# Optimization experiments

Hardware: AMD Instinct MI355X
Metric: run time of the kernel (lower is better)

The kernel has to match this reference:

```python
import jax, jax.numpy as jnp
import numpy as np

N, E, D, L = 50000, 800000, 128, 3  # nodes, edges, feature dim, layers
BN_EPS = 1e-5


def setup_inputs() -> dict:
    key = jax.random.key(0)
    ks = jax.random.split(key, 6)
    x = jax.random.normal(ks[0], (N, D), dtype=jnp.float32)
    edge_index = jax.random.randint(ks[1], (2, E), 0, N, dtype=jnp.int64)
    eps = jnp.zeros((L,), dtype=jnp.float32)
    # Linear weights ~ fan-in scaled init for numerical sanity
    W1 = jax.random.normal(ks[2], (L, D, D), dtype=jnp.float32) * (1.0 / np.sqrt(D))
    b1 = jnp.zeros((L, D), dtype=jnp.float32)
    W2 = jax.random.normal(ks[3], (L, D, D), dtype=jnp.float32) * (1.0 / np.sqrt(D))
    b2 = jnp.zeros((L, D), dtype=jnp.float32)
    bn1_g = jnp.ones((L, D), dtype=jnp.float32)
    bn1_b = jnp.zeros((L, D), dtype=jnp.float32)
    bn2_g = jnp.ones((L, D), dtype=jnp.float32)
    bn2_b = jnp.zeros((L, D), dtype=jnp.float32)
    return {"x": x, "edge_index": edge_index, "eps": eps, "W1": W1, "b1": b1,
            "bn1_g": bn1_g, "bn1_b": bn1_b, "W2": W2, "b2": b2,
            "bn2_g": bn2_g, "bn2_b": bn2_b}


def _batchnorm(h, g, b):
    # training-mode BatchNorm1d over node axis
    mu = h.mean(axis=0)
    var = h.var(axis=0)
    return (h - mu) * jax.lax.rsqrt(var + BN_EPS) * g + b


def reference(x, edge_index, eps, W1, b1, bn1_g, bn1_b, W2, b2, bn2_g, bn2_b):
    src = edge_index[0]
    dst = edge_index[1]
    h = x
    for l in range(L):
        # message: relu(x_j) gathered per edge; aggregate: scatter-add at dst
        agg = jax.ops.segment_sum(jax.nn.relu(h[src]), dst, num_segments=N)
        z = (1.0 + eps[l]) * h + agg
        # GINConv.mlp: Linear -> BN -> ReLU -> Linear
        z = _batchnorm(z @ W1[l] + b1[l], bn1_g[l], bn1_b[l])
        z = jax.nn.relu(z) @ W2[l] + b2[l]
        # outer per-layer BatchNorm
        z = _batchnorm(z, bn2_g[l], bn2_b[l])
        # ReLU on all but last layer (dropout is identity in eval)
        h = jax.nn.relu(z) if l < L - 1 else z
    return h
```

## Files before the change

kernel.cpp:

```cpp
#include <hip/hip_runtime.h>

#define N_NODES 50000
#define DIM 128
#define BN_EPS 1e-5f

__global__ __launch_bounds__(256) void edge_hist(const int* __restrict__ dst,
                                                 int* __restrict__ cnt, int E) {
  const int e = blockIdx.x * blockDim.x + threadIdx.x;
  if (e < E) atomicAdd(&cnt[dst[e]], 1);
}

__global__ __launch_bounds__(1024) void edge_scan(const int* __restrict__ cnt,
                                                  int* __restrict__ row_ptr) {
  __shared__ int part[1024];
  const int tid = threadIdx.x;
  const int per = (N_NODES + 1023) / 1024;
  const int start = tid * per;
  const int end = min(start + per, N_NODES);
  int s = 0;
  for (int i = start; i < end; ++i) s += cnt[i];
  part[tid] = s;
  __syncthreads();
  for (int off = 1; off < 1024; off <<= 1) {
    const int v = part[tid];
    const int u = (tid >= off) ? part[tid - off] : 0;
    __syncthreads();
    part[tid] = v + u;
    __syncthreads();
  }
  int run = (tid == 0) ? 0 : part[tid - 1];
  for (int i = start; i < end; ++i) {
    row_ptr[i] = run;
    run += cnt[i];
  }
  if (tid == 1023) row_ptr[N_NODES] = run;
}

__global__ __launch_bounds__(256) void edge_fill(const int* __restrict__ src,
                                                 const int* __restrict__ dst,
                                                 const int* __restrict__ row_ptr,
                                                 int* __restrict__ cur,
                                                 int* __restrict__ srcl, int E) {
  const int e = blockIdx.x * blockDim.x + threadIdx.x;
  if (e < E) {
    const int d = dst[e];
    const int pos = row_ptr[d] + atomicAdd(&cur[d], 1);
    srcl[pos] = src[e];
  }
}

template <int FUSE>
__global__ __launch_bounds__(256) void aggregate_combine(
    const float* __restrict__ h, const int* __restrict__ rp,
    const int* __restrict__ srcl, const float* __restrict__ eps_l,
    const float* __restrict__ ac, float* __restrict__ z) {
  const int node =
      __builtin_amdgcn_readfirstlane(blockIdx.x * 4 + (threadIdx.x >> 6));
  if (node >= N_NODES) return;
  const int lane = threadIdx.x & 63;
  const int col = lane * 2;

  float2 av, cv;
  if (FUSE) {
    av.x = ac[col]; av.y = ac[col + 1];
    cv.x = ac[DIM + col]; cv.y = ac[DIM + col + 1];
  }
  const float epsv = 1.0f + *eps_l;

  float2 acc;
  {
    const float2 u =
        *reinterpret_cast<const float2*>(h + (size_t)node * DIM + col);
    float2 s;
    if (FUSE) {
      s.x = fmaxf(fmaf(av.x, u.x, cv.x), 0.f);
      s.y = fmaxf(fmaf(av.y, u.y, cv.y), 0.f);
    } else {
      s = u;
    }
    acc.x = epsv * s.x;
    acc.y = epsv * s.y;
  }

  int p = rp[node];
  const int pe = rp[node + 1];
  for (; p + 8 <= pe; p += 8) {
    int s[8];
#pragma unroll
    for (int i = 0; i < 8; ++i) s[i] = srcl[p + i];
    float2 v[8];
#pragma unroll
    for (int i = 0; i < 8; ++i)
      v[i] = *reinterpret_cast<const float2*>(h + (size_t)s[i] * DIM + col);
#pragma unroll
    for (int i = 0; i < 8; ++i) {
      float mx, my;
      if (FUSE) {
        mx = fmaxf(fmaf(av.x, v[i].x, cv.x), 0.f);
        my = fmaxf(fmaf(av.y, v[i].y, cv.y), 0.f);
      } else {
        mx = fmaxf(v[i].x, 0.f);
        my = fmaxf(v[i].y, 0.f);
      }
      acc.x += mx;
      acc.y += my;
    }
  }
  for (; p < pe; ++p) {
    const int s = srcl[p];
    const float2 v =
        *reinterpret_cast<const float2*>(h + (size_t)s * DIM + col);
    if (FUSE) {
      acc.x += fmaxf(fmaf(av.x, v.x, cv.x), 0.f);
      acc.y += fmaxf(fmaf(av.y, v.y, cv.y), 0.f);
    } else {
      acc.x += fmaxf(v.x, 0.f);
      acc.y += fmaxf(v.y, 0.f);
    }
  }
  *reinterpret_cast<float2*>(z + (size_t)node * DIM + col) = acc;
}

template <int MODE>
__global__ __launch_bounds__(256) void gemm_rw(
    const float* __restrict__ in, const float* __restrict__ ac,
    const float* __restrict__ W, const float* __restrict__ bias,
    float* __restrict__ out, float* __restrict__ stats) {
  const int lane = threadIdx.x & 63;
  const int colb = __builtin_amdgcn_readfirstlane((threadIdx.x >> 6) * 32);
  const int row = blockIdx.x * 64 + lane;
  const bool valid = row < N_NODES;
  const float* __restrict__ zr = in + (size_t)(valid ? row : 0) * DIM;

  float acc[32];
#pragma unroll
  for (int j = 0; j < 32; ++j) acc[j] = 0.f;

#define LDCH(Z0, Z1, CH)                                                    \
  {                                                                         \
    const int kb_ = (CH) * 8;                                               \
    Z0 = *reinterpret_cast<const float4*>(zr + kb_);                        \
    Z1 = *reinterpret_cast<const float4*>(zr + kb_ + 4);                    \
    if (MODE == 1) {                                                        \
      const float4 A0_ = *reinterpret_cast<const float4*>(ac + kb_);        \
      const float4 A1_ = *reinterpret_cast<const float4*>(ac + kb_ + 4);    \
      const float4 C0_ = *reinterpret_cast<const float4*>(ac + DIM + kb_);  \
      const float4 C1_ = *reinterpret_cast<const float4*>(ac + DIM + kb_ + 4); \
      Z0.x = fmaxf(fmaf(A0_.x, Z0.x, C0_.x), 0.f);                          \
      Z0.y = fmaxf(fmaf(A0_.y, Z0.y, C0_.y), 0.f);                          \
      Z0.z = fmaxf(fmaf(A0_.z, Z0.z, C0_.z), 0.f);                          \
      Z0.w = fmaxf(fmaf(A0_.w, Z0.w, C0_.w), 0.f);                          \
      Z1.x = fmaxf(fmaf(A1_.x, Z1.x, C1_.x), 0.f);                          \
      Z1.y = fmaxf(fmaf(A1_.y, Z1.y, C1_.y), 0.f);                          \
      Z1.z = fmaxf(fmaf(A1_.z, Z1.z, C1_.z), 0.f);                          \
      Z1.w = fmaxf(fmaf(A1_.w, Z1.w, C1_.w), 0.f);                          \
    }                                                                       \
  }

#define FMAK(ZK, KG)                                                        \
  {                                                                         \
    const float* __restrict__ wk_ = W + (size_t)(KG)*DIM + colb;            \
    _Pragma("unroll") for (int j = 0; j < 32; ++j) acc[j] =                 \
        fmaf(wk_[j], (ZK), acc[j]);                                         \
  }

#define FMACH(Z0, Z1, CH)                                                   \
  {                                                                         \
    const int kb0_ = (CH) * 8;                                              \
    FMAK(Z0.x, kb0_ + 0) FMAK(Z0.y, kb0_ + 1)                               \
    FMAK(Z0.z, kb0_ + 2) FMAK(Z0.w, kb0_ + 3)                               \
    FMAK(Z1.x, kb0_ + 4) FMAK(Z1.y, kb0_ + 5)                               \
    FMAK(Z1.z, kb0_ + 6) FMAK(Z1.w, kb0_ + 7)                               \
  }

  float4 a0, a1, b0, b1;
  LDCH(a0, a1, 0)
#pragma unroll 1
  for (int c = 0; c < 16; c += 2) {
    LDCH(b0, b1, c + 1)
    FMACH(a0, a1, c)
    if (c + 2 < 16) LDCH(a0, a1, c + 2)
    FMACH(b0, b1, c + 1)
  }
#undef LDCH
#undef FMAK
#undef FMACH

  const float* __restrict__ bb = bias + colb;
  float v[32];
#pragma unroll
  for (int j = 0; j < 32; ++j) v[j] = valid ? (acc[j] + bb[j]) : 0.f;
  if (valid) {
    float* op = out + (size_t)row * DIM + colb;
#pragma unroll
    for (int j4 = 0; j4 < 8; ++j4) {
      float4 o;
      o.x = v[j4 * 4 + 0]; o.y = v[j4 * 4 + 1];
      o.z = v[j4 * 4 + 2]; o.w = v[j4 * 4 + 3];
      *reinterpret_cast<float4*>(op + j4 * 4) = o;
    }
  }
  float q[16];
#pragma unroll
  for (int jj = 0; jj < 16; ++jj) {
    const bool hi = (lane & 32) != 0;
    const float keep = hi ? v[jj + 16] : v[jj];
    const float send = hi ? v[jj] : v[jj + 16];
    const float recv = __shfl_xor(send, 32);
    v[jj] = keep + recv;
    q[jj] = keep * keep + recv * recv;
  }
#define RSTEP(ARR, CNT, O)                                                  \
  {                                                                         \
    _Pragma("unroll") for (int jj = 0; jj < (CNT); ++jj) {                  \
      const bool hi_ = (lane & (O)) != 0;                                   \
      const float keep_ = hi_ ? ARR[jj + (CNT)] : ARR[jj];                  \
      const float send_ = hi_ ? ARR[jj] : ARR[jj + (CNT)];                  \
      ARR[jj] = keep_ + __shfl_xor(send_, (O));                             \
    }                                                                       \
  }
  RSTEP(v, 8, 16) RSTEP(q, 8, 16)
  RSTEP(v, 4, 8)  RSTEP(q, 4, 8)
  RSTEP(v, 2, 4)  RSTEP(q, 2, 4)
  RSTEP(v, 1, 2)  RSTEP(q, 1, 2)
#undef RSTEP
  v[0] += __shfl_xor(v[0], 1);
  q[0] += __shfl_xor(q[0], 1);
  if ((lane & 1) == 0) {
    const int jc = colb + (lane >> 1);
    atomicAdd(&stats[jc], v[0]);
    atomicAdd(&stats[DIM + jc], q[0]);
  }
}

__global__ void bn_param(const float* __restrict__ stats,
                         const float* __restrict__ g,
                         const float* __restrict__ b, float* __restrict__ ac) {
  const int j = threadIdx.x;
  const float invN = 1.0f / (float)N_NODES;
  const float mu = stats[j] * invN;
  const float var = stats[DIM + j] * invN - mu * mu;
  const float a = g[j] * rsqrtf(var + BN_EPS);
  ac[j] = a;
  ac[DIM + j] = b[j] - mu * a;
}

__global__ __launch_bounds__(256) void apply_bn(const float* __restrict__ t,
                                                const float* __restrict__ ac,
                                                float* __restrict__ out) {
  const int i = blockIdx.x * blockDim.x + threadIdx.x;
  const int k = (i * 4) & (DIM - 1);
  const float4 v = *reinterpret_cast<const float4*>(&t[(size_t)i * 4]);
  const float4 a = *reinterpret_cast<const float4*>(&ac[k]);
  const float4 c = *reinterpret_cast<const float4*>(&ac[DIM + k]);
  float4 r;
  r.x = fmaf(a.x, v.x, c.x);
  r.y = fmaf(a.y, v.y, c.y);
  r.z = fmaf(a.z, v.z, c.z);
  r.w = fmaf(a.w, v.w, c.w);
  *reinterpret_cast<float4*>(&out[(size_t)i * 4]) = r;
}

extern "C" void kernel_launch(void* const* d_in, const int* in_sizes, int n_in,
                              void* d_out, int out_size, void* d_ws,
                              size_t ws_size, hipStream_t stream) {
  const float* x = (const float*)d_in[0];
  const int* ei = (const int*)d_in[1];
  const float* eps = (const float*)d_in[2];
  const float* W1 = (const float*)d_in[3];
  const float* b1 = (const float*)d_in[4];
  const float* g1 = (const float*)d_in[5];
  const float* bb1 = (const float*)d_in[6];
  const float* W2 = (const float*)d_in[7];
  const float* b2 = (const float*)d_in[8];
  const float* g2 = (const float*)d_in[9];
  const float* bb2 = (const float*)d_in[10];

  const int E = in_sizes[1] / 2;
  const size_t ND = (size_t)N_NODES * DIM;

  float* bufA = (float*)d_ws;
  float* bufB = bufA + ND;
  float* stats = bufB + ND;
  float* bnp = stats + 512;
  int* cnt = (int*)(bnp + 512);
  int* row_ptr = cnt + N_NODES;
  int* cur = row_ptr + N_NODES + 1;
  int* srcl = cur + N_NODES;

  const int edge_grid = (E + 255) / 256;
  const int agg_grid = (N_NODES + 3) / 4;
  const int gemm_grid = (N_NODES + 63) / 64;
  const int apply_grid = (N_NODES * DIM / 4) / 256;

  hipMemsetAsync(cnt, 0, sizeof(int) * (size_t)N_NODES, stream);
  hipMemsetAsync(cur, 0, sizeof(int) * (size_t)N_NODES, stream);
  edge_hist<<<edge_grid, 256, 0, stream>>>(ei + E, cnt, E);
  edge_scan<<<1, 1024, 0, stream>>>(cnt, row_ptr);
  edge_fill<<<edge_grid, 256, 0, stream>>>(ei, ei + E, row_ptr, cur, srcl, E);

  const float* hin = x;
  float* zb = bufA;
  float* tb = bufB;
  for (int l = 0; l < 3; ++l) {
    hipMemsetAsync(stats, 0, sizeof(float) * 512, stream);
    if (l == 0)
      aggregate_combine<0><<<agg_grid, 256, 0, stream>>>(hin, row_ptr, srcl,
                                                         eps + l, nullptr, zb);
    else
      aggregate_combine<1><<<agg_grid, 256, 0, stream>>>(
          hin, row_ptr, srcl, eps + l, bnp + 256, zb);
    gemm_rw<2><<<gemm_grid, 256, 0, stream>>>(
        zb, nullptr, W1 + (size_t)l * DIM * DIM, b1 + l * DIM, tb, stats);
    bn_param<<<1, DIM, 0, stream>>>(stats, g1 + l * DIM, bb1 + l * DIM, bnp);
    gemm_rw<1><<<gemm_grid, 256, 0, stream>>>(
        tb, bnp, W2 + (size_t)l * DIM * DIM, b2 + l * DIM, zb, stats + 256);
    bn_param<<<1, DIM, 0, stream>>>(stats + 256, g2 + l * DIM, bb2 + l * DIM,
                                    bnp + 256);
    hin = zb;
    float* tmp = zb;
    zb = tb;
    tb = tmp;
  }
  apply_bn<<<apply_grid, 256, 0, stream>>>(hin, bnp + 256, (float*)d_out);
}
```

Before: 883.7 us.

## Stage GEMM weights in LDS and compute two rows per thread

The dense 128x128 GEMM kernel now copies the full weight matrix into shared memory once per block. Each thread computes two output rows (128 rows per block) instead of one, so every weight read from LDS is reused across two rows. The per-column BN statistics reduction is restructured to add the two rows' contributions before the cross-lane shuffle reduction. This is meant to cut the scalar and global weight loads per FMA, at the cost of 64KB LDS per block (lower occupancy) and more registers from two 32-wide accumulators.

After: 1.650 ms. 86.7% more time.

```diff
diff --git a/kernel.cpp b/kernel.cpp
--- a/kernel.cpp
+++ b/kernel.cpp
@@ -122,113 +122,148 @@
 }
 
 template <int MODE>
-__global__ __launch_bounds__(256) void gemm_rw(
+__global__ __launch_bounds__(256) void gemm_v3(
     const float* __restrict__ in, const float* __restrict__ ac,
     const float* __restrict__ W, const float* __restrict__ bias,
     float* __restrict__ out, float* __restrict__ stats) {
-  const int lane = threadIdx.x & 63;
-  const int colb = __builtin_amdgcn_readfirstlane((threadIdx.x >> 6) * 32);
-  const int row = blockIdx.x * 64 + lane;
-  const bool valid = row < N_NODES;
-  const float* __restrict__ zr = in + (size_t)(valid ? row : 0) * DIM;
-
-  float acc[32];
-#pragma unroll
-  for (int j = 0; j < 32; ++j) acc[j] = 0.f;
-
-#define LDCH(Z0, Z1, CH)                                                    \
-  {                                                                         \
-    const int kb_ = (CH) * 8;                                               \
-    Z0 = *reinterpret_cast<const float4*>(zr + kb_);                        \
-    Z1 = *reinterpret_cast<const float4*>(zr + kb_ + 4);                    \
-    if (MODE == 1) {                                                        \
-      const float4 A0_ = *reinterpret_cast<const float4*>(ac + kb_);        \
-      const float4 A1_ = *reinterpret_cast<const float4*>(ac + kb_ + 4);    \
-      const float4 C0_ = *reinterpret_cast<const float4*>(ac + DIM + kb_);  \
-      const float4 C1_ = *reinterpret_cast<const float4*>(ac + DIM + kb_ + 4); \
-      Z0.x = fmaxf(fmaf(A0_.x, Z0.x, C0_.x), 0.f);                          \
-      Z0.y = fmaxf(fmaf(A0_.y, Z0.y, C0_.y), 0.f);                          \
-      Z0.z = fmaxf(fmaf(A0_.z, Z0.z, C0_.z), 0.f);                          \
-      Z0.w = fmaxf(fmaf(A0_.w, Z0.w, C0_.w), 0.f);                          \
-      Z1.x = fmaxf(fmaf(A1_.x, Z1.x, C1_.x), 0.f);                          \
-      Z1.y = fmaxf(fmaf(A1_.y, Z1.y, C1_.y), 0.f);                          \
-      Z1.z = fmaxf(fmaf(A1_.z, Z1.z, C1_.z), 0.f);                          \
-      Z1.w = fmaxf(fmaf(A1_.w, Z1.w, C1_.w), 0.f);                          \
-    }                                                                       \
-  }
-
-#define FMAK(ZK, KG)                                                        \
-  {                                                                         \
-    const float* __restrict__ wk_ = W + (size_t)(KG)*DIM + colb;            \
-    _Pragma("unroll") for (int j = 0; j < 32; ++j) acc[j] =                 \
-        fmaf(wk_[j], (ZK), acc[j]);                                         \
-  }
-
-#define FMACH(Z0, Z1, CH)                                                   \
-  {                                                                         \
-    const int kb0_ = (CH) * 8;                                              \
-    FMAK(Z0.x, kb0_ + 0) FMAK(Z0.y, kb0_ + 1)                               \
-    FMAK(Z0.z, kb0_ + 2) FMAK(Z0.w, kb0_ + 3)                               \
-    FMAK(Z1.x, kb0_ + 4) FMAK(Z1.y, kb0_ + 5)                               \
-    FMAK(Z1.z, kb0_ + 6) FMAK(Z1.w, kb0_ + 7)                               \
-  }
-
-  float4 a0, a1, b0, b1;
-  LDCH(a0, a1, 0)
+  __shared__ float w_lds[DIM * DIM];
+
+  const int tid = threadIdx.x;
+  const int lane = tid & 63;
+  const int colb = __builtin_amdgcn_readfirstlane((tid >> 6) * 32);
+  const int r0 = blockIdx.x * 128 + lane;
+  const int r1 = r0 + 64;
+  const bool v0 = r0 < N_NODES;
+  const bool v1 = r1 < N_NODES;
+  const float* __restrict__ zp0 = in + (size_t)(v0 ? r0 : 0) * DIM;
+  const float* __restrict__ zp1 = in + (size_t)(v1 ? r1 : 0) * DIM;
+
+  float acc0[32], acc1[32];
+#pragma unroll
+  for (int j = 0; j < 32; ++j) { acc0[j] = 0.f; acc1[j] = 0.f; }
+
+#define LOADZ(Z0, Z1, C)                                                     \
+  {                                                                          \
+    const int kb_ = (C) * 16;                                                \
+    _Pragma("unroll") for (int q = 0; q < 4; ++q) {                          \
+      Z0[q] = *reinterpret_cast<const float4*>(zp0 + kb_ + q * 4);           \
+      Z1[q] = *reinterpret_cast<const float4*>(zp1 + kb_ + q * 4);           \
+      if (MODE == 1) {                                                       \
+        const float4 A_ = *reinterpret_cast<const float4*>(ac + kb_ + q * 4);\
+        const float4 C_ =                                                    \
+            *reinterpret_cast<const float4*>(ac + DIM + kb_ + q * 4);        \
+        Z0[q].x = fmaxf(fmaf(A_.x, Z0[q].x, C_.x), 0.f);                     \
+        Z0[q].y = fmaxf(fmaf(A_.y, Z0[q].y, C_.y), 0.f);                     \
+        Z0[q].z = fmaxf(fmaf(A_.z, Z0[q].z, C_.z), 0.f);                     \
+        Z0[q].w = fmaxf(fmaf(A_.w, Z0[q].w, C_.w), 0.f);                     \
+        Z1[q].x = fmaxf(fmaf(A_.x, Z1[q].x, C_.x), 0.f);                     \
+        Z1[q].y = fmaxf(fmaf(A_.y, Z1[q].y, C_.y), 0.f);                     \
+        Z1[q].z = fmaxf(fmaf(A_.z, Z1[q].z, C_.z), 0.f);                     \
+        Z1[q].w = fmaxf(fmaf(A_.w, Z1[q].w, C_.w), 0.f);                     \
+      }                                                                      \
+    }                                                                        \
+  }
+
+#define FMA_K(z0v, z1v, KIDX)                                                \
+  {                                                                          \
+    _Pragma("unroll") for (int jj = 0; jj < 8; ++jj) {                       \
+      const float4 wf_ = *reinterpret_cast<const float4*>(                   \
+          &w_lds[(KIDX) * DIM + colb + jj * 4]);                             \
+      acc0[jj * 4 + 0] = fmaf(wf_.x, (z0v), acc0[jj * 4 + 0]);               \
+      acc0[jj * 4 + 1] = fmaf(wf_.y, (z0v), acc0[jj * 4 + 1]);               \
+      acc0[jj * 4 + 2] = fmaf(wf_.z, (z0v), acc0[jj * 4 + 2]);               \
+      acc0[jj * 4 + 3] = fmaf(wf_.w, (z0v), acc0[jj * 4 + 3]);               \
+      acc1[jj * 4 + 0] = fmaf(wf_.x, (z1v), acc1[jj * 4 + 0]);               \
+      acc1[jj * 4 + 1] = fmaf(wf_.y, (z1v), acc1[jj * 4 + 1]);               \
+      acc1[jj * 4 + 2] = fmaf(wf_.z, (z1v), acc1[jj * 4 + 2]);               \
+      acc1[jj * 4 + 3] = fmaf(wf_.w, (z1v), acc1[jj * 4 + 3]);               \
+    }                                                                        \
+  }
+
+#define COMPUTE(Z0, Z1, C)                                                   \
+  {                                                                          \
+    _Pragma("unroll") for (int q = 0; q < 4; ++q) {                          \
+      const int k0_ = (C) * 16 + q * 4;                                      \
+      FMA_K(Z0[q].x, Z1[q].x, k0_ + 0)                                       \
+      FMA_K(Z0[q].y, Z1[q].y, k0_ + 1)                                       \
+      FMA_K(Z0[q].z, Z1[q].z, k0_ + 2)                                       \
+      FMA_K(Z0[q].w, Z1[q].w, k0_ + 3)                                       \
+    }                                                                        \
+  }
+
+  float4 xa0[4], xa1[4], xb0[4], xb1[4];
+  LOADZ(xa0, xa1, 0)
+
+#pragma unroll
+  for (int it = 0; it < 16; ++it) {
+    const int i4 = it * 256 + tid;
+    *reinterpret_cast<float4*>(&w_lds[i4 * 4]) =
+        *reinterpret_cast<const float4*>(&W[(size_t)i4 * 4]);
+  }
+  __syncthreads();
+
 #pragma unroll 1
-  for (int c = 0; c < 16; c += 2) {
-    LDCH(b0, b1, c + 1)
-    FMACH(a0, a1, c)
-    if (c + 2 < 16) LDCH(a0, a1, c + 2)
-    FMACH(b0, b1, c + 1)
-  }
-#undef LDCH
-#undef FMAK
-#undef FMACH
+  for (int c = 0; c < 8; c += 2) {
+    LOADZ(xb0, xb1, c + 1)
+    COMPUTE(xa0, xa1, c)
+    if (c + 2 < 8) LOADZ(xa0, xa1, c + 2)
+    COMPUTE(xb0, xb1, c + 1)
+  }
+#undef LOADZ
+#undef FMA_K
+#undef COMPUTE
 
   const float* __restrict__ bb = bias + colb;
-  float v[32];
-#pragma unroll
-  for (int j = 0; j < 32; ++j) v[j] = valid ? (acc[j] + bb[j]) : 0.f;
-  if (valid) {
-    float* op = out + (size_t)row * DIM + colb;
+  float s[32], q[32];
+#pragma unroll
+  for (int j = 0; j < 32; ++j) {
+    const float x0 = v0 ? (acc0[j] + bb[j]) : 0.f;
+    const float x1 = v1 ? (acc1[j] + bb[j]) : 0.f;
+    acc0[j] = x0;
+    acc1[j] = x1;
+    s[j] = x0 + x1;
+    q[j] = x0 * x0 + x1 * x1;
+  }
+  if (v0) {
+    float* op = out + (size_t)r0 * DIM + colb;
 #pragma unroll
     for (int j4 = 0; j4 < 8; ++j4) {
       float4 o;
-      o.x = v[j4 * 4 + 0]; o.y = v[j4 * 4 + 1];
-      o.z = v[j4 * 4 + 2]; o.w = v[j4 * 4 + 3];
+      o.x = acc0[j4 * 4 + 0]; o.y = acc0[j4 * 4 + 1];
+      o.z = acc0[j4 * 4 + 2]; o.w = acc0[j4 * 4 + 3];
       *reinterpret_cast<float4*>(op + j4 * 4) = o;
     }
   }
-  float q[16];
-#pragma unroll
-  for (int jj = 0; jj < 16; ++jj) {
-    const bool hi = (lane & 32) != 0;
-    const float keep = hi ? v[jj + 16] : v[jj];
-    const float send = hi ? v[jj] : v[jj + 16];
-    const float recv = __shfl_xor(send, 32);
-    v[jj] = keep + recv;
-    q[jj] = keep * keep + recv * recv;
-  }
-#define RSTEP(ARR, CNT, O)                                                  \
-  {                                                                         \
-    _Pragma("unroll") for (int jj = 0; jj < (CNT); ++jj) {                  \
-      const bool hi_ = (lane & (O)) != 0;                                   \
-      const float keep_ = hi_ ? ARR[jj + (CNT)] : ARR[jj];                  \
-      const float send_ = hi_ ? ARR[jj] : ARR[jj + (CNT)];                  \
-      ARR[jj] = keep_ + __shfl_xor(send_, (O));                             \
-    }                                                                       \
-  }
-  RSTEP(v, 8, 16) RSTEP(q, 8, 16)
-  RSTEP(v, 4, 8)  RSTEP(q, 4, 8)
-  RSTEP(v, 2, 4)  RSTEP(q, 2, 4)
-  RSTEP(v, 1, 2)  RSTEP(q, 1, 2)
+  if (v1) {
+    float* op = out + (size_t)r1 * DIM + colb;
+#pragma unroll
+    for (int j4 = 0; j4 < 8; ++j4) {
+      float4 o;
+      o.x = acc1[j4 * 4 + 0]; o.y = acc1[j4 * 4 + 1];
+      o.z = acc1[j4 * 4 + 2]; o.w = acc1[j4 * 4 + 3];
+      *reinterpret_cast<float4*>(op + j4 * 4) = o;
+    }
+  }
+#define RSTEP(ARR, CNT, O)                                                   \
+  {                                                                          \
+    _Pragma("unroll") for (int jj = 0; jj < (CNT); ++jj) {                   \
+      const bool hi_ = (lane & (O)) != 0;                                    \
+      const float keep_ = hi_ ? ARR[jj + (CNT)] : ARR[jj];                   \
+      const float send_ = hi_ ? ARR[jj] : ARR[jj + (CNT)];                   \
+      ARR[jj] = keep_ + __shfl_xor(send_, (O));                              \
+    }                                                                        \
+  }
+  RSTEP(s, 16, 32) RSTEP(q, 16, 32)
+  RSTEP(s, 8, 16)  RSTEP(q, 8, 16)
+  RSTEP(s, 4, 8)   RSTEP(q, 4, 8)
+  RSTEP(s, 2, 4)   RSTEP(q, 2, 4)
+  RSTEP(s, 1, 2)   RSTEP(q, 1, 2)
 #undef RSTEP
-  v[0] += __shfl_xor(v[0], 1);
+  s[0] += __shfl_xor(s[0], 1);
   q[0] += __shfl_xor(q[0], 1);
   if ((lane & 1) == 0) {
     const int jc = colb + (lane >> 1);
-    atomicAdd(&stats[jc], v[0]);
+    atomicAdd(&stats[jc], s[0]);
     atomicAdd(&stats[DIM + jc], q[0]);
   }
 }
@@ -290,7 +325,7 @@
 
   const int edge_grid = (E + 255) / 256;
   const int agg_grid = (N_NODES + 3) / 4;
-  const int gemm_grid = (N_NODES + 63) / 64;
+  const int gemm_grid = (N_NODES + 127) / 128;
   const int apply_grid = (N_NODES * DIM / 4) / 256;
 
   hipMemsetAsync(cnt, 0, sizeof(int) * (size_t)N_NODES, stream);
@@ -310,10 +345,10 @@
     else
       aggregate_combine<1><<<agg_grid, 256, 0, stream>>>(
           hin, row_ptr, srcl, eps + l, bnp + 256, zb);
-    gemm_rw<2><<<gemm_grid, 256, 0, stream>>>(
+    gemm_v3<2><<<gemm_grid, 256, 0, stream>>>(
         zb, nullptr, W1 + (size_t)l * DIM * DIM, b1 + l * DIM, tb, stats);
     bn_param<<<1, DIM, 0, stream>>>(stats, g1 + l * DIM, bb1 + l * DIM, bnp);
-    gemm_rw<1><<<gemm_grid, 256, 0, stream>>>(
+    gemm_v3<1><<<gemm_grid, 256, 0, stream>>>(
         tb, bnp, W2 + (size_t)l * DIM * DIM, b2 + l * DIM, zb, stats + 256);
     bn_param<<<1, DIM, 0, stream>>>(stats + 256, g2 + l * DIM, bb2 + l * DIM,
                                     bnp + 256);
```

## Replace FP32 FMA GEMM with split-bf16 MFMA GEMM using prepacked weights

Applied to the files above, without the earlier changes.

Swaps the scalar FP32 FMA matrix multiply for one built on the bf16 MFMA 16x16x32 instructions. Precision is kept near FP32 by splitting each operand into bf16 hi and lo parts and issuing three MFMAs (hi*hi, lo*hi, hi*lo). Weights are split and repacked into the MFMA fragment layout by a new prep kernel once per call. The epilogue writes output, adds bias, and accumulates the BatchNorm column sums and squared sums through shuffles and atomics. The cost is three times the MFMA work, a per-element conversion step, and small accuracy differences from the dropped lo*lo term.

New measurement: 834.2 us. 5.6% less time.

```diff
diff --git a/kernel.cpp b/kernel.cpp
--- a/kernel.cpp
+++ b/kernel.cpp
@@ -3,6 +3,18 @@
 #define N_NODES 50000
 #define DIM 128
 #define BN_EPS 1e-5f
+
+typedef short bf16x8 __attribute__((ext_vector_type(8)));
+typedef float f32x4 __attribute__((ext_vector_type(4)));
+
+__device__ __forceinline__ unsigned short f2bf(float x) {
+  unsigned u = __float_as_uint(x);
+  u += 0x7FFFu + ((u >> 16) & 1u);
+  return (unsigned short)(u >> 16);
+}
+__device__ __forceinline__ float bf2f(unsigned short h) {
+  return __uint_as_float(((unsigned)h) << 16);
+}
 
 __global__ __launch_bounds__(256) void edge_hist(const int* __restrict__ dst,
                                                  int* __restrict__ cnt, int E) {
@@ -121,115 +133,144 @@
   *reinterpret_cast<float2*>(z + (size_t)node * DIM + col) = acc;
 }
 
+__global__ __launch_bounds__(256) void prep_w(const float* __restrict__ W,
+                                              unsigned short* __restrict__ hi,
+                                              unsigned short* __restrict__ lo) {
+  const int idx = blockIdx.x * 256 + threadIdx.x;
+  const int i = idx & 7;
+  const int l = (idx >> 3) & 63;
+  const int t = (idx >> 9) & 7;
+  const int s = idx >> 12;
+  const int k = s * 32 + ((l >> 4) << 3) + i;
+  const int j = t * 16 + (l & 15);
+  const float v = W[k * DIM + j];
+  const unsigned short h = f2bf(v);
+  hi[idx] = h;
+  lo[idx] = f2bf(v - bf2f(h));
+}
+
 template <int MODE>
-__global__ __launch_bounds__(256) void gemm_rw(
+__global__ __launch_bounds__(256, 2) void gemm_mfma(
     const float* __restrict__ in, const float* __restrict__ ac,
-    const float* __restrict__ W, const float* __restrict__ bias,
+    const unsigned short* __restrict__ whi,
+    const unsigned short* __restrict__ wlo, const float* __restrict__ bias,
     float* __restrict__ out, float* __restrict__ stats) {
-  const int lane = threadIdx.x & 63;
-  const int colb = __builtin_amdgcn_readfirstlane((threadIdx.x >> 6) * 32);
-  const int row = blockIdx.x * 64 + lane;
-  const bool valid = row < N_NODES;
-  const float* __restrict__ zr = in + (size_t)(valid ? row : 0) * DIM;
-
-  float acc[32];
-#pragma unroll
-  for (int j = 0; j < 32; ++j) acc[j] = 0.f;
-
-#define LDCH(Z0, Z1, CH)                                                    \
-  {                                                                         \
-    const int kb_ = (CH) * 8;                                               \
-    Z0 = *reinterpret_cast<const float4*>(zr + kb_);                        \
-    Z1 = *reinterpret_cast<const float4*>(zr + kb_ + 4);                    \
-    if (MODE == 1) {                                                        \
-      const float4 A0_ = *reinterpret_cast<const float4*>(ac + kb_);        \
-      const float4 A1_ = *reinterpret_cast<const float4*>(ac + kb_ + 4);    \
-      const float4 C0_ = *reinterpret_cast<const float4*>(ac + DIM + kb_);  \
-      const float4 C1_ = *reinterpret_cast<const float4*>(ac + DIM + kb_ + 4); \
-      Z0.x = fmaxf(fmaf(A0_.x, Z0.x, C0_.x), 0.f);                          \
-      Z0.y = fmaxf(fmaf(A0_.y, Z0.y, C0_.y), 0.f);                          \
-      Z0.z = fmaxf(fmaf(A0_.z, Z0.z, C0_.z), 0.f);                          \
-      Z0.w = fmaxf(fmaf(A0_.w, Z0.w, C0_.w), 0.f);                          \
-      Z1.x = fmaxf(fmaf(A1_.x, Z1.x, C1_.x), 0.f);                          \
-      Z1.y = fmaxf(fmaf(A1_.y, Z1.y, C1_.y), 0.f);                          \
-      Z1.z = fmaxf(fmaf(A1_.z, Z1.z, C1_.z), 0.f);                          \
-      Z1.w = fmaxf(fmaf(A1_.w, Z1.w, C1_.w), 0.f);                          \
-    }                                                                       \
-  }
-
-#define FMAK(ZK, KG)                                                        \
-  {                                                                         \
-    const float* __restrict__ wk_ = W + (size_t)(KG)*DIM + colb;            \
-    _Pragma("unroll") for (int j = 0; j < 32; ++j) acc[j] =                 \
-        fmaf(wk_[j], (ZK), acc[j]);                                         \
-  }
-
-#define FMACH(Z0, Z1, CH)                                                   \
-  {                                                                         \
-    const int kb0_ = (CH) * 8;                                              \
-    FMAK(Z0.x, kb0_ + 0) FMAK(Z0.y, kb0_ + 1)                               \
-    FMAK(Z0.z, kb0_ + 2) FMAK(Z0.w, kb0_ + 3)                               \
-    FMAK(Z1.x, kb0_ + 4) FMAK(Z1.y, kb0_ + 5)                               \
-    FMAK(Z1.z, kb0_ + 6) FMAK(Z1.w, kb0_ + 7)                               \
-  }
-
-  float4 a0, a1, b0, b1;
-  LDCH(a0, a1, 0)
+  const int tid = threadIdx.x;
+  const int lane = tid & 63;
+  const int wv = tid >> 6;
+  const int rbase = blockIdx.x * 128 + wv * 32;
+  const int lr = lane & 15;
+  const int lk = (lane >> 4) << 3;
+
+  f32x4 acc[2][8];
+#pragma unroll
+  for (int m = 0; m < 2; ++m)
+#pragma unroll
+    for (int t = 0; t < 8; ++t) acc[m][t] = (f32x4)(0.f);
+
+  const int r0 = min(rbase + lr, N_NODES - 1);
+  const int r1 = min(rbase + 16 + lr, N_NODES - 1);
+  const float* __restrict__ z0 = in + (size_t)r0 * DIM + lk;
+  const float* __restrict__ z1 = in + (size_t)r1 * DIM + lk;
+  const bf16x8* __restrict__ bh = (const bf16x8*)whi + lane;
+  const bf16x8* __restrict__ bl = (const bf16x8*)wlo + lane;
+
 #pragma unroll 1
-  for (int c = 0; c < 16; c += 2) {
-    LDCH(b0, b1, c + 1)
-    FMACH(a0, a1, c)
-    if (c + 2 < 16) LDCH(a0, a1, c + 2)
-    FMACH(b0, b1, c + 1)
-  }
-#undef LDCH
-#undef FMAK
-#undef FMACH
-
-  const float* __restrict__ bb = bias + colb;
-  float v[32];
-#pragma unroll
-  for (int j = 0; j < 32; ++j) v[j] = valid ? (acc[j] + bb[j]) : 0.f;
-  if (valid) {
-    float* op = out + (size_t)row * DIM + colb;
-#pragma unroll
-    for (int j4 = 0; j4 < 8; ++j4) {
-      float4 o;
-      o.x = v[j4 * 4 + 0]; o.y = v[j4 * 4 + 1];
-      o.z = v[j4 * 4 + 2]; o.w = v[j4 * 4 + 3];
-      *reinterpret_cast<float4*>(op + j4 * 4) = o;
-    }
-  }
-  float q[16];
-#pragma unroll
-  for (int jj = 0; jj < 16; ++jj) {
-    const bool hi = (lane & 32) != 0;
-    const float keep = hi ? v[jj + 16] : v[jj];
-    const float send = hi ? v[jj] : v[jj + 16];
-    const float recv = __shfl_xor(send, 32);
-    v[jj] = keep + recv;
-    q[jj] = keep * keep + recv * recv;
-  }
-#define RSTEP(ARR, CNT, O)                                                  \
-  {                                                                         \
-    _Pragma("unroll") for (int jj = 0; jj < (CNT); ++jj) {                  \
-      const bool hi_ = (lane & (O)) != 0;                                   \
-      const float keep_ = hi_ ? ARR[jj + (CNT)] : ARR[jj];                  \
-      const float send_ = hi_ ? ARR[jj] : ARR[jj + (CNT)];                  \
-      ARR[jj] = keep_ + __shfl_xor(send_, (O));                             \
-    }                                                                       \
-  }
-  RSTEP(v, 8, 16) RSTEP(q, 8, 16)
-  RSTEP(v, 4, 8)  RSTEP(q, 4, 8)
-  RSTEP(v, 2, 4)  RSTEP(q, 2, 4)
-  RSTEP(v, 1, 2)  RSTEP(q, 1, 2)
-#undef RSTEP
-  v[0] += __shfl_xor(v[0], 1);
-  q[0] += __shfl_xor(q[0], 1);
-  if ((lane & 1) == 0) {
-    const int jc = colb + (lane >> 1);
-    atomicAdd(&stats[jc], v[0]);
-    atomicAdd(&stats[DIM + jc], q[0]);
+  for (int s = 0; s < 4; ++s) {
+    const int k0 = s * 32;
+    float a0v[8], a1v[8];
+    {
+      const float4 p0 = *reinterpret_cast<const float4*>(z0 + k0);
+      const float4 p1 = *reinterpret_cast<const float4*>(z0 + k0 + 4);
+      a0v[0] = p0.x; a0v[1] = p0.y; a0v[2] = p0.z; a0v[3] = p0.w;
+      a0v[4] = p1.x; a0v[5] = p1.y; a0v[6] = p1.z; a0v[7] = p1.w;
+      const float4 q0 = *reinterpret_cast<const float4*>(z1 + k0);
+      const float4 q1 = *reinterpret_cast<const float4*>(z1 + k0 + 4);
+      a1v[0] = q0.x; a1v[1] = q0.y; a1v[2] = q0.z; a1v[3] = q0.w;
+      a1v[4] = q1.x; a1v[5] = q1.y; a1v[6] = q1.z; a1v[7] = q1.w;
+    }
+    if (MODE == 1) {
+      const float4 A0 = *reinterpret_cast<const float4*>(ac + k0 + lk);
+      const float4 A1 = *reinterpret_cast<const float4*>(ac + k0 + lk + 4);
+      const float4 C0 = *reinterpret_cast<const float4*>(ac + DIM + k0 + lk);
+      const float4 C1 =
+          *reinterpret_cast<const float4*>(ac + DIM + k0 + lk + 4);
+      float aa[8], cc[8];
+      aa[0] = A0.x; aa[1] = A0.y; aa[2] = A0.z; aa[3] = A0.w;
+      aa[4] = A1.x; aa[5] = A1.y; aa[6] = A1.z; aa[7] = A1.w;
+      cc[0] = C0.x; cc[1] = C0.y; cc[2] = C0.z; cc[3] = C0.w;
+      cc[4] = C1.x; cc[5] = C1.y; cc[6] = C1.z; cc[7] = C1.w;
+#pragma unroll
+      for (int i = 0; i < 8; ++i) {
+        a0v[i] = fmaxf(fmaf(aa[i], a0v[i], cc[i]), 0.f);
+        a1v[i] = fmaxf(fmaf(aa[i], a1v[i], cc[i]), 0.f);
+      }
+    }
+    bf16x8 ah0, al0, ah1, al1;
+#pragma unroll
+    for (int i = 0; i < 8; ++i) {
+      unsigned short h = f2bf(a0v[i]);
+      ah0[i] = (short)h;
+      al0[i] = (short)f2bf(a0v[i] - bf2f(h));
+      h = f2bf(a1v[i]);
+      ah1[i] = (short)h;
+      al1[i] = (short)f2bf(a1v[i] - bf2f(h));
+    }
+#pragma unroll
+    for (int t = 0; t < 8; ++t) {
+      const bf16x8 bhv = bh[(s * 8 + t) * 64];
+      const bf16x8 blv = bl[(s * 8 + t) * 64];
+      acc[0][t] =
+          __builtin_amdgcn_mfma_f32_16x16x32_bf16(ah0, bhv, acc[0][t], 0, 0, 0);
+      acc[0][t] =
+          __builtin_amdgcn_mfma_f32_16x16x32_bf16(al0, bhv, acc[0][t], 0, 0, 0);
+      acc[0][t] =
+          __builtin_amdgcn_mfma_f32_16x16x32_bf16(ah0, blv, acc[0][t], 0, 0, 0);
+      acc[1][t] =
+          __builtin_amdgcn_mfma_f32_16x16x32_bf16(ah1, bhv, acc[1][t], 0, 0, 0);
+      acc[1][t] =
+          __builtin_amdgcn_mfma_f32_16x16x32_bf16(al1, bhv, acc[1][t], 0, 0, 0);
+      acc[1][t] =
+          __builtin_amdgcn_mfma_f32_16x16x32_bf16(ah1, blv, acc[1][t], 0, 0, 0);
+    }
+  }
+
+  float bj[8];
+#pragma unroll
+  for (int t = 0; t < 8; ++t) bj[t] = bias[t * 16 + lr];
+  float cs[8], cq[8];
+#pragma unroll
+  for (int t = 0; t < 8; ++t) { cs[t] = 0.f; cq[t] = 0.f; }
+#pragma unroll
+  for (int m = 0; m < 2; ++m) {
+    const int rb2 = rbase + m * 16 + ((lane >> 4) << 2);
+#pragma unroll
+    for (int t = 0; t < 8; ++t) {
+#pragma unroll
+      for (int j = 0; j < 4; ++j) {
+        const int rr = rb2 + j;
+        const float v = acc[m][t][j] + bj[t];
+        if (rr < N_NODES) {
+          out[(size_t)rr * DIM + t * 16 + lr] = v;
+          cs[t] += v;
+          cq[t] += v * v;
+        }
+      }
+    }
+  }
+#pragma unroll
+  for (int t = 0; t < 8; ++t) {
+    cs[t] += __shfl_xor(cs[t], 16);
+    cs[t] += __shfl_xor(cs[t], 32);
+    cq[t] += __shfl_xor(cq[t], 16);
+    cq[t] += __shfl_xor(cq[t], 32);
+  }
+  if (lane < 16) {
+#pragma unroll
+    for (int t = 0; t < 8; ++t) {
+      atomicAdd(&stats[t * 16 + lane], cs[t]);
+      atomicAdd(&stats[DIM + t * 16 + lane], cq[t]);
+    }
   }
 }
 
@@ -287,11 +328,19 @@
   int* row_ptr = cnt + N_NODES;
   int* cur = row_ptr + N_NODES + 1;
   int* srcl = cur + N_NODES;
+  unsigned short* wf = (unsigned short*)(srcl + E);
 
   const int edge_grid = (E + 255) / 256;
   const int agg_grid = (N_NODES + 3) / 4;
-  const int gemm_grid = (N_NODES + 63) / 64;
+  const int gemm_grid = (N_NODES + 127) / 128;
   const int apply_grid = (N_NODES * DIM / 4) / 256;
+
+  for (int l = 0; l < 3; ++l) {
+    unsigned short* f1 = wf + (size_t)(2 * l) * 32768;
+    unsigned short* f2 = wf + (size_t)(2 * l + 1) * 32768;
+    prep_w<<<64, 256, 0, stream>>>(W1 + (size_t)l * DIM * DIM, f1, f1 + 16384);
+    prep_w<<<64, 256, 0, stream>>>(W2 + (size_t)l * DIM * DIM, f2, f2 + 16384);
+  }
 
   hipMemsetAsync(cnt, 0, sizeof(int) * (size_t)N_NODES, stream);
   hipMemsetAsync(cur, 0, sizeof(int) * (size_t)N_NODES, stream);
@@ -303,6 +352,8 @@
   float* zb = bufA;
   float* tb = bufB;
   for (int l = 0; l < 3; ++l) {
+    unsigned short* f1 = wf + (size_t)(2 * l) * 32768;
+    unsigned short* f2 = wf + (size_t)(2 * l + 1) * 32768;
     hipMemsetAsync(stats, 0, sizeof(float) * 512, stream);
     if (l == 0)
       aggregate_combine<0><<<agg_grid, 256, 0, stream>>>(hin, row_ptr, srcl,
@@ -310,11 +361,11 @@
     else
       aggregate_combine<1><<<agg_grid, 256, 0, stream>>>(
           hin, row_ptr, srcl, eps + l, bnp + 256, zb);
-    gemm_rw<2><<<gemm_grid, 256, 0, stream>>>(
-        zb, nullptr, W1 + (size_t)l * DIM * DIM, b1 + l * DIM, tb, stats);
+    gemm_mfma<2><<<gemm_grid, 256, 0, stream>>>(zb, nullptr, f1, f1 + 16384,
+                                                b1 + l * DIM, tb, stats);
     bn_param<<<1, DIM, 0, stream>>>(stats, g1 + l * DIM, bb1 + l * DIM, bnp);
-    gemm_rw<1><<<gemm_grid, 256, 0, stream>>>(
-        tb, bnp, W2 + (size_t)l * DIM * DIM, b2 + l * DIM, zb, stats + 256);
+    gemm_mfma<1><<<gemm_grid, 256, 0, stream>>>(tb, bnp, f2, f2 + 16384,
+                                                b2 + l * DIM, zb, stats + 256);
     bn_param<<<1, DIM, 0, stream>>>(stats + 256, g2 + l * DIM, bb2 + l * DIM,
                                     bnp + 256);
     hin = zb;
```
